# Optimization experiments

Hardware: AMD Instinct MI355X
Metric: run time of the kernel (lower is better)

The kernel has to match this reference:

```python
import jax, jax.numpy as jnp
import numpy as np
from jax import lax

ROI_H = 8        # _ROI_HEIGHT
MAX_BOX = 32     # generator.MAX_BOX
MAX_LEN = 64     # static cap on pooled width/height (replaces dynamic max_width)
SCALE = 8.0      # feature_map_scale
IOU_THR = 0.5    # tf.image.non_max_suppression default
SCORE_THR = 0.3
B, H, W, C = 4, 64, 64, 128


def _reconstruct_boxes(b, scale):
    # b: [B,H,W,4] per-pixel (l,t,r,b) offsets -> absolute (x1,y1,x2,y2) * scale
    Hd, Wd = b.shape[1], b.shape[2]
    xx = jnp.arange(Wd, dtype=b.dtype)[None, None, :]
    yy = jnp.arange(Hd, dtype=b.dtype)[None, :, None]
    left = xx - b[..., 0]
    top = yy - b[..., 1]
    right = xx + b[..., 2]
    bottom = yy + b[..., 3]
    return scale * jnp.stack([left, top, right, bottom], axis=-1)


def _nms_single(bbs, ss):
    # greedy NMS, bbs: [N,4] (x1,y1,x2,y2), ss: [N]; returns [MAX_BOX,4]
    x1, y1, x2, y2 = bbs[:, 0], bbs[:, 1], bbs[:, 2], bbs[:, 3]
    areas = (x2 - x1) * (y2 - y1)

    def body(i, state):
        valid, sel = state
        m = jnp.where(valid, ss, -jnp.inf)
        j = jnp.argmax(m)
        ok = m[j] > -jnp.inf
        sel = sel.at[i].set(jnp.where(ok, j.astype(jnp.int32), -1))
        bj = bbs[j]
        iw = jnp.maximum(jnp.minimum(x2, bj[2]) - jnp.maximum(x1, bj[0]), 0.0)
        ih = jnp.maximum(jnp.minimum(y2, bj[3]) - jnp.maximum(y1, bj[1]), 0.0)
        inter = iw * ih
        iou = inter / (areas + areas[j] - inter + 1e-9)
        valid = valid & (iou <= IOU_THR)   # selected box self-suppresses (iou=1)
        return valid, sel

    N = bbs.shape[0]
    valid0 = jnp.ones((N,), dtype=bool)
    sel0 = jnp.full((MAX_BOX,), -1, dtype=jnp.int32)
    _, sel = lax.fori_loop(0, MAX_BOX, body, (valid0, sel0))
    ok = sel >= 0
    idx = jnp.maximum(sel, 0)
    sb = bbs[idx]
    sc = ss[idx]
    keep = ok & (sc >= SCORE_THR)
    return jnp.where(keep[:, None], sb, jnp.zeros_like(sb))


def _bilinear(img, x, y):
    # img [H,W,C], x [Wp], y [Hp] -> [Hp,Wp,C]; matches TF clip-then-weight behavior
    Hh, Ww = img.shape[0], img.shape[1]
    x0f = jnp.floor(x)
    y0f = jnp.floor(y)
    x0 = jnp.clip(x0f.astype(jnp.int32), 0, Ww - 1)
    x1 = jnp.clip(x0f.astype(jnp.int32) + 1, 0, Ww - 1)
    y0 = jnp.clip(y0f.astype(jnp.int32), 0, Hh - 1)
    y1 = jnp.clip(y0f.astype(jnp.int32) + 1, 0, Hh - 1)
    Ia = img[y0[:, None], x0[None, :]]
    Ib = img[y0[:, None], x1[None, :]]
    Ic = img[y1[:, None], x0[None, :]]
    Id = img[y1[:, None], x1[None, :]]
    x0v, x1v = x0.astype(img.dtype), x1.astype(img.dtype)
    y0v, y1v = y0.astype(img.dtype), y1.astype(img.dtype)
    wa = (x1v - x)[None, :] * (y1v - y)[:, None]
    wb = (x1v - x)[None, :] * (y - y0v)[:, None]
    wc = (x - x0v)[None, :] * (y1v - y)[:, None]
    wd = (x - x0v)[None, :] * (y - y0v)[:, None]
    return (Ia * wa[..., None] + Ib * wb[..., None]
            + Ic * wc[..., None] + Id * wd[..., None])


def _pool_one(img, box, horizontal):
    # img [H,W,C], box [4] in feature-map coords
    w = box[2] - box[0]
    h = box[3] - box[1]
    is_dir = (w >= h) if horizontal else (w < h)
    bz = jnp.where(is_dir, box, jnp.zeros_like(box))
    w = bz[2] - bz[0]
    h = bz[3] - bz[1]
    non_zero = (w >= 0.1) | (h >= 0.1)
    bw = jnp.where(w <= 0.0, 1e-4, w)
    bh = jnp.where(h <= 0.0, 1e-4, h)
    ratio = jnp.where(non_zero, (bw / bh) if horizontal else (bh / bw), 0.0)
    n = jnp.minimum(jnp.ceil(ratio * ROI_H), float(MAX_LEN)).astype(jnp.int32)
    length_f = jnp.maximum(n.astype(img.dtype), 2.0)  # guard div-by-zero for masked boxes
    fmask = non_zero.astype(img.dtype)
    if horizontal:
        map_w = bw / (length_f - 1.0)
        map_h = bh / (ROI_H - 1.0)
        xx = jnp.arange(MAX_LEN, dtype=img.dtype) * map_w + bz[0]
        yy = jnp.arange(ROI_H, dtype=img.dtype) * map_h + bz[1]
        pooled = _bilinear(img, xx, yy)                     # [ROI_H, MAX_LEN, C]
        colmask = (jnp.arange(MAX_LEN) < n).astype(img.dtype) * fmask
        pooled = pooled * colmask[None, :, None]
    else:
        map_w = bw / (ROI_H - 1.0)
        map_h = bh / (length_f - 1.0)
        xx = jnp.arange(ROI_H, dtype=img.dtype) * map_w + bz[0]
        yy = jnp.arange(MAX_LEN, dtype=img.dtype) * map_h + bz[1]
        pooled = _bilinear(img, xx, yy)                     # [MAX_LEN, ROI_H, C]
        rowmask = (jnp.arange(MAX_LEN) < n).astype(img.dtype) * fmask
        pooled = pooled * rowmask[:, None, None]
    return pooled, n


def _roi_pool(fmap, boxes, horizontal):
    # fmap [B,H,W,C], boxes [B,M,4] -> ([B,M,...], [B,M])
    per_img = lambda img, bxs: jax.vmap(lambda b: _pool_one(img, b, horizontal))(bxs)
    return jax.vmap(per_img)(fmap, boxes)


def setup_inputs() -> dict:
    key = jax.random.key(0)
    k1, k2 = jax.random.split(key)
    fmap = jax.random.normal(k1, (B, H, W, C), dtype=jnp.float32)
    # channel 0 -> score logit, channels 1:5 -> positive l/t/r/b offsets in fmap px
    bbox_output = jax.random.uniform(k2, (B, H, W, 5), dtype=jnp.float32) * 3.0
    return {"fmap": fmap, "bbox_output": bbox_output}


def reference(fmap, bbox_output):
    scores = jax.nn.sigmoid(bbox_output[..., 0])                  # [B,H,W]
    boxes = _reconstruct_boxes(bbox_output[..., 1:5], SCALE)      # [B,H,W,4]
    Bn = scores.shape[0]
    bbs = boxes.reshape(Bn, -1, 4)
    ss = scores.reshape(Bn, -1)
    nms_boxes = jax.vmap(_nms_single)(bbs, ss)                    # [B,MAX_BOX,4]
    fb = nms_boxes / SCALE                                        # back to fmap coords
    h_roi, widths = _roi_pool(fmap, fb, True)    # [B,M,8,MAX_LEN,C], [B,M]
    v_roi, heights = _roi_pool(fmap, fb, False)  # [B,M,MAX_LEN,8,C], [B,M]
    return nms_boxes, h_roi, widths, v_roi, heights
```

## Files before the change

### kernel.cpp

```cpp
#include <hip/hip_runtime.h>
#include <hip/hip_bf16.h>
#include <math.h>

#pragma clang fp contract(off)

#define NPIX 4096
#define MAXB 32
#define NB   4
#define ROI_N 8388608
#define OTOT (ROI_N / 8)

__global__ __launch_bounds__(256) void nms_kernel(const float* __restrict__ bbox,
                                                  float* __restrict__ out_nms,
                                                  float* __restrict__ params,
                                                  float* __restrict__ out_w,
                                                  float* __restrict__ out_hh)
{
    const int b = blockIdx.x;
    const int t = threadIdx.x;

    __shared__ float s_box[NPIX][4];
    __shared__ float s_sel[MAXB][4];
    __shared__ float s_red[2][4][2];

    float rs[16], rx1[16], ry1[16], rx2[16], ry2[16], rar[16];

    const float* src = bbox + (size_t)b * NPIX * 5;

    #pragma unroll
    for (int i = 0; i < 16; ++i) {
        int p = i * 256 + t;
        int y = p >> 6, x = p & 63;
        float c0 = src[p * 5 + 0];
        float c1 = src[p * 5 + 1];
        float c2 = src[p * 5 + 2];
        float c3 = src[p * 5 + 3];
        float c4 = src[p * 5 + 4];
        float sc = 1.0f / (1.0f + expf(-c0));
        float x1 = 8.0f * ((float)x - c1);
        float y1 = 8.0f * ((float)y - c2);
        float x2 = 8.0f * ((float)x + c3);
        float y2 = 8.0f * ((float)y + c4);
        rs[i] = sc;
        rx1[i] = x1; ry1[i] = y1; rx2[i] = x2; ry2[i] = y2;
        rar[i] = (x2 - x1) * (y2 - y1);
        s_box[p][0] = x1; s_box[p][1] = y1; s_box[p][2] = x2; s_box[p][3] = y2;
    }
    __syncthreads();

    unsigned valid = 0xFFFFu;
    float wx1 = -1e30f, wy1 = -1e30f, wx2 = -1e30f, wy2 = -1e30f, warea = 0.f;

    for (int it = 0; it < MAXB; ++it) {
        float best = -INFINITY;
        int   bidx = 0x7FFFFFFF;
        #pragma unroll
        for (int i = 0; i < 16; ++i) {
            float iw = fmaxf(fminf(rx2[i], wx2) - fmaxf(rx1[i], wx1), 0.f);
            float ih = fmaxf(fminf(ry2[i], wy2) - fmaxf(ry1[i], wy1), 0.f);
            float inter = iw * ih;
            float iou = __fdiv_rn(inter, rar[i] + warea - inter + 1e-9f);
            valid &= ~(((iou > 0.5f) ? 1u : 0u) << i);
            float vv = ((valid >> i) & 1u) ? rs[i] : -INFINITY;
            bool take = vv > best;
            bidx = take ? (i * 256 + t) : bidx;
            best = take ? vv : best;
        }
        #pragma unroll
        for (int off = 32; off; off >>= 1) {
            float ov = __shfl_xor(best, off);
            int   oi = __shfl_xor(bidx, off);
            bool take = (ov > best) || (ov == best && oi < bidx);
            best = take ? ov : best;
            bidx = take ? oi : bidx;
        }
        int buf = it & 1;
        if ((t & 63) == 0) {
            s_red[buf][t >> 6][0] = best;
            s_red[buf][t >> 6][1] = __int_as_float(bidx);
        }
        __syncthreads();
        best = s_red[buf][0][0]; bidx = __float_as_int(s_red[buf][0][1]);
        #pragma unroll
        for (int wv = 1; wv < 4; ++wv) {
            float ov = s_red[buf][wv][0];
            int   oi = __float_as_int(s_red[buf][wv][1]);
            bool take = (ov > best) || (ov == best && oi < bidx);
            best = take ? ov : best;
            bidx = take ? oi : bidx;
        }

        int jj = min(bidx, NPIX - 1);
        wx1 = s_box[jj][0]; wy1 = s_box[jj][1];
        wx2 = s_box[jj][2]; wy2 = s_box[jj][3];
        warea = (wx2 - wx1) * (wy2 - wy1);

        if (t == 0) {
            bool keep = (best >= 0.3f);
            float o0 = keep ? wx1 : 0.f, o1 = keep ? wy1 : 0.f;
            float o2 = keep ? wx2 : 0.f, o3 = keep ? wy2 : 0.f;
            float* o = out_nms + ((size_t)b * MAXB + it) * 4;
            o[0] = o0; o[1] = o1; o[2] = o2; o[3] = o3;
            s_sel[it][0] = o0; s_sel[it][1] = o1;
            s_sel[it][2] = o2; s_sel[it][3] = o3;
        }
    }
    __syncthreads();

    if (t < 64) {
        int dir = t >> 5, bx = t & 31;
        float x1 = s_sel[bx][0] * 0.125f, y1 = s_sel[bx][1] * 0.125f;
        float x2 = s_sel[bx][2] * 0.125f, y2 = s_sel[bx][3] * 0.125f;
        float w = x2 - x1, h = y2 - y1;
        bool is_dir = (dir == 0) ? (w >= h) : (w < h);
        if (!is_dir) { x1 = 0.f; y1 = 0.f; x2 = 0.f; y2 = 0.f; }
        w = x2 - x1; h = y2 - y1;
        bool  non_zero = (w >= 0.1f) || (h >= 0.1f);
        float bw = (w <= 0.f) ? 1e-4f : w;
        float bh = (h <= 0.f) ? 1e-4f : h;
        float ratio = non_zero ? ((dir == 0) ? __fdiv_rn(bw, bh) : __fdiv_rn(bh, bw)) : 0.f;
        int   n = (int)fminf(ceilf(ratio * 8.0f), 64.0f);
        float length_f = fmaxf((float)n, 2.0f);
        float fmask = non_zero ? 1.f : 0.f;
        float map_w, map_h;
        if (dir == 0) { map_w = __fdiv_rn(bw, length_f - 1.0f); map_h = __fdiv_rn(bh, 7.0f); }
        else          { map_w = __fdiv_rn(bw, 7.0f);            map_h = __fdiv_rn(bh, length_f - 1.0f); }
        int gtb = b * MAXB + bx;
        float* P = params + ((size_t)dir * 128 + gtb) * 8;
        P[0] = x1; P[1] = y1; P[2] = map_w; P[3] = map_h;
        P[4] = (float)n; P[5] = fmask; P[6] = 0.f; P[7] = 0.f;
        ((dir == 0) ? out_w : out_hh)[gtb] = (float)n;
    }
}

__global__ __launch_bounds__(256) void roi_kernel(const float* __restrict__ fmap,
                                                  const float* __restrict__ params,
                                                  float* __restrict__ out_h,
                                                  float* __restrict__ out_v)
{
    int idx = blockIdx.x * 256 + threadIdx.x;
    int dir = (idx >= OTOT) ? 1 : 0;
    int e   = idx - dir * OTOT;
    int tb  = e >> 13;
    int within = e & 8191;
    int pos = within >> 4;
    int ch8 = within & 15;

    const float4* P4 = (const float4*)(params + ((size_t)dir * 128 + tb) * 8);
    float4 p0 = P4[0];
    float4 p1 = P4[1];
    float bz0x = p0.x, bz0y = p0.y, map_w = p0.z, map_h = p0.w;
    int   n     = (int)p1.x;
    float fmask = p1.y;

    int rr, cc; float mask;
    if (dir == 0) { rr = pos >> 6; cc = pos & 63; mask = (cc < n) ? fmask : 0.f; }
    else          { rr = pos >> 3; cc = pos & 7;  mask = (rr < n) ? fmask : 0.f; }

    int el = (tb << 16) | (pos << 7) | (ch8 << 3);
    float* outp = ((dir == 0) ? out_h : out_v) + el;

    if (mask == 0.f) {
        float4 z = make_float4(0.f, 0.f, 0.f, 0.f);
        *(float4*)outp = z;
        *(float4*)(outp + 4) = z;
        return;
    }

    float x = __fadd_rn(__fmul_rn((float)cc, map_w), bz0x);
    float y = __fadd_rn(__fmul_rn((float)rr, map_h), bz0y);

    float x0f = floorf(x), y0f = floorf(y);
    int ix0 = min(max((int)x0f,     0), 63);
    int ix1 = min(max((int)x0f + 1, 0), 63);
    int iy0 = min(max((int)y0f,     0), 63);
    int iy1 = min(max((int)y0f + 1, 0), 63);

    const float* img = fmap + ((size_t)(tb >> 5)) * (64 * 64 * 128) + (ch8 << 3);
    const float* pa = img + (iy0 * 64 + ix0) * 128;
    const float* pb = img + (iy0 * 64 + ix1) * 128;
    const float* pc = img + (iy1 * 64 + ix0) * 128;
    const float* pd = img + (iy1 * 64 + ix1) * 128;
    float4 Ia0 = *(const float4*)pa,       Ia1 = *(const float4*)(pa + 4);
    float4 Ib0 = *(const float4*)pb,       Ib1 = *(const float4*)(pb + 4);
    float4 Ic0 = *(const float4*)pc,       Ic1 = *(const float4*)(pc + 4);
    float4 Id0 = *(const float4*)pd,       Id1 = *(const float4*)(pd + 4);

    float x0v = (float)ix0, x1v = (float)ix1;
    float y0v = (float)iy0, y1v = (float)iy1;
    float wa = (x1v - x) * (y1v - y);
    float wb = (x1v - x) * (y - y0v);
    float wc = (x - x0v) * (y1v - y);
    float wd = (x - x0v) * (y - y0v);

    float4 o0, o1;
    o0.x = (Ia0.x * wa + Ib0.x * wb + Ic0.x * wc + Id0.x * wd) * mask;
    o0.y = (Ia0.y * wa + Ib0.y * wb + Ic0.y * wc + Id0.y * wd) * mask;
    o0.z = (Ia0.z * wa + Ib0.z * wb + Ic0.z * wc + Id0.z * wd) * mask;
    o0.w = (Ia0.w * wa + Ib0.w * wb + Ic0.w * wc + Id0.w * wd) * mask;
    o1.x = (Ia1.x * wa + Ib1.x * wb + Ic1.x * wc + Id1.x * wd) * mask;
    o1.y = (Ia1.y * wa + Ib1.y * wb + Ic1.y * wc + Id1.y * wd) * mask;
    o1.z = (Ia1.z * wa + Ib1.z * wb + Ic1.z * wc + Id1.z * wd) * mask;
    o1.w = (Ia1.w * wa + Ib1.w * wb + Ic1.w * wc + Id1.w * wd) * mask;
    *(float4*)outp = o0;
    *(float4*)(outp + 4) = o1;
}

extern "C" void kernel_launch(void* const* d_in, const int* in_sizes, int n_in,
                              void* d_out, int out_size, void* d_ws, size_t ws_size,
                              hipStream_t stream) {
    const float* fmap = (const float*)d_in[0];
    const float* bbox = (const float*)d_in[1];
    float* out = (float*)d_out;

    float* out_nms = out;
    float* out_h   = out + 512;
    float* out_w   = out_h + ROI_N;
    float* out_v   = out_w + 128;
    float* out_hh  = out_v + ROI_N;

    float* params = (float*)d_ws;

    nms_kernel<<<NB, 256, 0, stream>>>(bbox, out_nms, params, out_w, out_hh);
    roi_kernel<<<(2 * OTOT) / 256, 256, 0, stream>>>(fmap, params, out_h, out_v);
}
```

Measured before the change: 139.6 us.

## Widen NMS block to 512 threads and use nontemporal stores in ROI pooling

The NMS kernel now runs 512 threads per image, so each thread holds 8 candidate boxes instead of 16 and the cross-wave reduction covers 8 waves. The ROI kernel takes its per-box parameters from the block index, which makes them uniform scalar loads, and writes its large outputs with nontemporal stores to avoid polluting the cache. The trade-off is more barrier and reduction work per NMS iteration, with the aim of cheaper output writes across the 64 MB of pooled results.

```diff
diff --git a/kernel.cpp b/kernel.cpp
--- a/kernel.cpp
+++ b/kernel.cpp
@@ -8,9 +8,10 @@
 #define MAXB 32
 #define NB   4
 #define ROI_N 8388608
-#define OTOT (ROI_N / 8)
-
-__global__ __launch_bounds__(256) void nms_kernel(const float* __restrict__ bbox,
+
+typedef float f32x4 __attribute__((ext_vector_type(4)));
+
+__global__ __launch_bounds__(512) void nms_kernel(const float* __restrict__ bbox,
                                                   float* __restrict__ out_nms,
                                                   float* __restrict__ params,
                                                   float* __restrict__ out_w,
@@ -21,15 +22,15 @@
 
     __shared__ float s_box[NPIX][4];
     __shared__ float s_sel[MAXB][4];
-    __shared__ float s_red[2][4][2];
-
-    float rs[16], rx1[16], ry1[16], rx2[16], ry2[16], rar[16];
+    __shared__ float s_red[2][8][2];
+
+    float rs[8], rx1[8], ry1[8], rx2[8], ry2[8], rar[8];
 
     const float* src = bbox + (size_t)b * NPIX * 5;
 
     #pragma unroll
-    for (int i = 0; i < 16; ++i) {
-        int p = i * 256 + t;
+    for (int i = 0; i < 8; ++i) {
+        int p = i * 512 + t;
         int y = p >> 6, x = p & 63;
         float c0 = src[p * 5 + 0];
         float c1 = src[p * 5 + 1];
@@ -48,14 +49,14 @@
     }
     __syncthreads();
 
-    unsigned valid = 0xFFFFu;
+    unsigned valid = 0xFFu;
     float wx1 = -1e30f, wy1 = -1e30f, wx2 = -1e30f, wy2 = -1e30f, warea = 0.f;
 
     for (int it = 0; it < MAXB; ++it) {
         float best = -INFINITY;
         int   bidx = 0x7FFFFFFF;
         #pragma unroll
-        for (int i = 0; i < 16; ++i) {
+        for (int i = 0; i < 8; ++i) {
             float iw = fmaxf(fminf(rx2[i], wx2) - fmaxf(rx1[i], wx1), 0.f);
             float ih = fmaxf(fminf(ry2[i], wy2) - fmaxf(ry1[i], wy1), 0.f);
             float inter = iw * ih;
@@ -63,7 +64,7 @@
             valid &= ~(((iou > 0.5f) ? 1u : 0u) << i);
             float vv = ((valid >> i) & 1u) ? rs[i] : -INFINITY;
             bool take = vv > best;
-            bidx = take ? (i * 256 + t) : bidx;
+            bidx = take ? (i * 512 + t) : bidx;
             best = take ? vv : best;
         }
         #pragma unroll
@@ -82,7 +83,7 @@
         __syncthreads();
         best = s_red[buf][0][0]; bidx = __float_as_int(s_red[buf][0][1]);
         #pragma unroll
-        for (int wv = 1; wv < 4; ++wv) {
+        for (int wv = 1; wv < 8; ++wv) {
             float ov = s_red[buf][wv][0];
             int   oi = __float_as_int(s_red[buf][wv][1]);
             bool take = (ov > best) || (ov == best && oi < bidx);
@@ -138,20 +139,20 @@
                                                   float* __restrict__ out_h,
                                                   float* __restrict__ out_v)
 {
-    int idx = blockIdx.x * 256 + threadIdx.x;
-    int dir = (idx >= OTOT) ? 1 : 0;
-    int e   = idx - dir * OTOT;
-    int tb  = e >> 13;
-    int within = e & 8191;
-    int pos = within >> 4;
-    int ch8 = within & 15;
-
-    const float4* P4 = (const float4*)(params + ((size_t)dir * 128 + tb) * 8);
-    float4 p0 = P4[0];
-    float4 p1 = P4[1];
-    float bz0x = p0.x, bz0y = p0.y, map_w = p0.z, map_h = p0.w;
-    int   n     = (int)p1.x;
-    float fmask = p1.y;
+    int blk = blockIdx.x;
+    int dir = (blk >= 4096) ? 1 : 0;
+    int bb  = blk - dir * 4096;
+    int tb  = bb >> 5;
+    int sub = bb & 31;
+
+    const float* P = params + ((size_t)(dir * 128 + tb)) * 8;
+    float bz0x = P[0], bz0y = P[1], map_w = P[2], map_h = P[3];
+    int   n     = (int)P[4];
+    float fmask = P[5];
+
+    int item = (sub << 8) | threadIdx.x;
+    int pos  = item >> 4;
+    int ch8  = item & 15;
 
     int rr, cc; float mask;
     if (dir == 0) { rr = pos >> 6; cc = pos & 63; mask = (cc < n) ? fmask : 0.f; }
@@ -161,9 +162,9 @@
     float* outp = ((dir == 0) ? out_h : out_v) + el;
 
     if (mask == 0.f) {
-        float4 z = make_float4(0.f, 0.f, 0.f, 0.f);
-        *(float4*)outp = z;
-        *(float4*)(outp + 4) = z;
+        f32x4 z = (f32x4)(0.f);
+        __builtin_nontemporal_store(z, (f32x4*)outp);
+        __builtin_nontemporal_store(z, (f32x4*)(outp + 4));
         return;
     }
 
@@ -181,10 +182,10 @@
     const float* pb = img + (iy0 * 64 + ix1) * 128;
     const float* pc = img + (iy1 * 64 + ix0) * 128;
     const float* pd = img + (iy1 * 64 + ix1) * 128;
-    float4 Ia0 = *(const float4*)pa,       Ia1 = *(const float4*)(pa + 4);
-    float4 Ib0 = *(const float4*)pb,       Ib1 = *(const float4*)(pb + 4);
-    float4 Ic0 = *(const float4*)pc,       Ic1 = *(const float4*)(pc + 4);
-    float4 Id0 = *(const float4*)pd,       Id1 = *(const float4*)(pd + 4);
+    f32x4 Ia0 = *(const f32x4*)pa,       Ia1 = *(const f32x4*)(pa + 4);
+    f32x4 Ib0 = *(const f32x4*)pb,       Ib1 = *(const f32x4*)(pb + 4);
+    f32x4 Ic0 = *(const f32x4*)pc,       Ic1 = *(const f32x4*)(pc + 4);
+    f32x4 Id0 = *(const f32x4*)pd,       Id1 = *(const f32x4*)(pd + 4);
 
     float x0v = (float)ix0, x1v = (float)ix1;
     float y0v = (float)iy0, y1v = (float)iy1;
@@ -193,7 +194,7 @@
     float wc = (x - x0v) * (y1v - y);
     float wd = (x - x0v) * (y - y0v);
 
-    float4 o0, o1;
+    f32x4 o0, o1;
     o0.x = (Ia0.x * wa + Ib0.x * wb + Ic0.x * wc + Id0.x * wd) * mask;
     o0.y = (Ia0.y * wa + Ib0.y * wb + Ic0.y * wc + Id0.y * wd) * mask;
     o0.z = (Ia0.z * wa + Ib0.z * wb + Ic0.z * wc + Id0.z * wd) * mask;
@@ -202,8 +203,8 @@
     o1.y = (Ia1.y * wa + Ib1.y * wb + Ic1.y * wc + Id1.y * wd) * mask;
     o1.z = (Ia1.z * wa + Ib1.z * wb + Ic1.z * wc + Id1.z * wd) * mask;
     o1.w = (Ia1.w * wa + Ib1.w * wb + Ic1.w * wc + Id1.w * wd) * mask;
-    *(float4*)outp = o0;
-    *(float4*)(outp + 4) = o1;
+    __builtin_nontemporal_store(o0, (f32x4*)outp);
+    __builtin_nontemporal_store(o1, (f32x4*)(outp + 4));
 }
 
 extern "C" void kernel_launch(void* const* d_in, const int* in_sizes, int n_in,
@@ -221,6 +222,6 @@
 
     float* params = (float*)d_ws;
 
-    nms_kernel<<<NB, 256, 0, stream>>>(bbox, out_nms, params, out_w, out_hh);
-    roi_kernel<<<(2 * OTOT) / 256, 256, 0, stream>>>(fmap, params, out_h, out_v);
+    nms_kernel<<<NB, 512, 0, stream>>>(bbox, out_nms, params, out_w, out_hh);
+    roi_kernel<<<8192, 256, 0, stream>>>(fmap, params, out_h, out_v);
 }
```

Result: no change. 141.9 us (+1.7%).
